# Kernel optimization log

Hardware: AMD Instinct MI355X
Metric: run time of the kernel (lower is better)

## Reference

```python
import jax, jax.numpy as jnp
import numpy as np
from jax import lax

DT = 1.0 / 120.0
B, T = 4096, 128
TWO_PI = 2.0 * np.pi


def setup_inputs() -> dict:
    key = jax.random.key(0)
    k1, k2, k3, k4 = jax.random.split(key, 4)
    return {
        "params": jax.random.normal(k1, (4,), jnp.float32),
        "covariance_params": jax.random.normal(k2, (7,), jnp.float32),
        "init_states": jax.random.normal(k3, (B, 6), jnp.float32),
        "measurements": jax.random.normal(k4, (B, T, 3), jnp.float32),
    }


def _wrap(a):
    # wrap angle innovation to [-pi, pi]
    return a - TWO_PI * jnp.round(a / TWO_PI)


def _smooth_loss(params, covariance_params, init_state, z):
    # z: [T, 3] measurements of (x, y, theta)
    friction = (jnp.tanh(params[0]) + 1.0) * 0.01
    damping = (jnp.tanh(params[1]) + 1.0) * 0.01
    cp = jax.nn.sigmoid(covariance_params)
    R = jnp.diag(cp[:3])                                    # [3,3] meas noise
    Q = jnp.diag(cp[jnp.array([3, 3, 4, 4, 5, 6])])         # [6,6] proc noise
    I6 = jnp.eye(6, dtype=z.dtype)
    Hm = jnp.zeros((3, 6), z.dtype).at[0, 0].set(1.).at[1, 1].set(1.).at[2, 4].set(1.)
    P0 = 0.01 * I6

    def f_and_F(s):
        # free-sliding puck dynamics: [x, y, dx, dy, th, dth]
        x, y, dx, dy, th, dth = s
        ndx = dx - DT * (damping * dx + friction * jnp.tanh(100. * dx))
        ndy = dy - DT * (damping * dy + friction * jnp.tanh(100. * dy))
        ndth = dth * (1.0 - DT * damping)
        ns = jnp.stack([x + DT * dx, y + DT * dy, ndx, ndy, th + DT * dth, ndth])
        gx = 1.0 - DT * (damping + friction * 100. * (1. - jnp.tanh(100. * dx) ** 2))
        gy = 1.0 - DT * (damping + friction * 100. * (1. - jnp.tanh(100. * dy) ** 2))
        F = (I6.at[0, 2].set(DT).at[1, 3].set(DT).at[4, 5].set(DT)
               .at[2, 2].set(gx).at[3, 3].set(gy).at[5, 5].set(1.0 - DT * damping))
        return ns, F

    def ekf_step(carry, zt):
        s, P = carry
        sp, F = f_and_F(s)
        Pp = F @ P @ F.T + Q
        S = Hm @ Pp @ Hm.T + R
        innov = zt - Hm @ sp
        innov = innov.at[2].set(_wrap(innov[2]))
        K = jnp.linalg.solve(S, Hm @ Pp).T          # Pp H^T S^-1
        s_new = sp + K @ innov
        P_new = (I6 - K @ Hm) @ Pp
        return (s_new, P_new), (s_new, P_new, sp, Pp, F)

    _, (sf, Pf, sp, Pp, Fs) = lax.scan(ekf_step, (init_state, P0), z)

    # RTS backward pass
    def rts_step(carry, inp):
        s_next, P_next = carry
        s_f, P_f, sp_n, Pp_n, F_n = inp
        G = jnp.linalg.solve(Pp_n, F_n @ P_f).T     # P_f F^T Pp^{-1}
        s_s = s_f + G @ (s_next - sp_n)
        P_s = P_f + G @ (P_next - Pp_n) @ G.T
        return (s_s, P_s), (s_s, P_s)

    inp = (sf[:-1], Pf[:-1], sp[1:], Pp[1:], Fs[1:])
    _, (s_sm_head, P_sm_head) = lax.scan(rts_step, (sf[-1], Pf[-1]), inp, reverse=True)
    s_sm = jnp.concatenate([s_sm_head, sf[-1:]], 0)   # [T,6]
    P_sm = jnp.concatenate([P_sm_head, Pf[-1:]], 0)   # [T,6,6]

    # log-lik style loss vs measurements[2:] (as in compute_loss)
    zz, st, Pt = z[2:], s_sm[2:], P_sm[2:]
    Sv = jnp.einsum('ij,tjk,lk->til', Hm, Pt, Hm) + R  # [T-2,3,3] meas-space var
    innov_xy = zz[:, :2] - st[:, :2]
    a = zz[:, 2] - st[:, 4]
    a = jnp.where(a > 1.5 * np.pi, a - TWO_PI, a)
    a = jnp.where(a < -1.5 * np.pi, a + TWO_PI, a)
    innov = jnp.concatenate([innov_xy, a[:, None]], 1)
    sign, logdet = jnp.linalg.slogdet(Sv)
    return jnp.sum(sign * jnp.exp(logdet) + jnp.einsum('ti,tij,tj->t', innov, Sv, innov))


def reference(params, covariance_params, init_states, measurements):
    per_seg = jax.vmap(_smooth_loss, in_axes=(None, None, 0, 0))(
        params, covariance_params, init_states, measurements)
    return jnp.sum(per_seg)
```

## Files before the change

kernel.cpp:

```cpp
#include <hip/hip_runtime.h>
#include <cmath>


namespace {

constexpr int B = 4096;
constexpr int T = 128;
constexpr int NT = B * 3;
constexpr int CPB = 64;
constexpr int NBLK = NT / CPB;
constexpr int RBLK = 512;
constexpr int RTH = 256;

constexpr float DTc     = 1.0f / 120.0f;
constexpr float TWO_PIc = 6.28318530717958647692f;
constexpr float PI_1_5  = 4.71238898038468985769f;
constexpr float INV_2PI = 0.15915494309189533577f;

__device__ __forceinline__ float frcp(float x) { return __builtin_amdgcn_rcpf(x); }

__device__ __forceinline__ float fast_tanh(float x) {
  float e = __expf(2.0f * x);
  return 1.0f - 2.0f * frcp(e + 1.0f);
}
__device__ __forceinline__ float sigmoidf(float x) {
  return frcp(1.0f + __expf(-x));
}

__global__ __launch_bounds__(256) void ztrans_kernel(
    const float* __restrict__ z, float* __restrict__ zt) {
  __shared__ float tile[96 * 65];
  const int tid = threadIdx.x;
  const int bs = blockIdx.x & 63;
  const int bt = blockIdx.x >> 6;
  const int s0 = bs * 64, t0 = bt * 32;

  const float* __restrict__ zbase = z + (size_t)s0 * 384 + t0 * 3;
#pragma unroll
  for (int k = 0; k < 6; k++) {
    const int idx = tid + k * 256;
    const int sl = idx / 24;
    const int c4 = idx - sl * 24;
    const float4 v4 = *(const float4*)(zbase + (size_t)sl * 384 + c4 * 4);
    tile[(c4 * 4 + 0) * 65 + sl] = v4.x;
    tile[(c4 * 4 + 1) * 65 + sl] = v4.y;
    tile[(c4 * 4 + 2) * 65 + sl] = v4.z;
    tile[(c4 * 4 + 3) * 65 + sl] = v4.w;
  }
  __syncthreads();
#pragma unroll
  for (int k = 0; k < 24; k++) {
    const int idx = tid + k * 256;
    const int r  = idx >> 6;
    const int sl = idx & 63;
    const int fc = r >> 5;
    const int tl = r & 31;
    zt[((size_t)fc * T + t0 + tl) * B + s0 + sl] = tile[(tl * 3 + fc) * 65 + sl];
  }
}

__global__ __launch_bounds__(CPB, 1) void filt_kernel(
    const float* __restrict__ params, const float* __restrict__ covp,
    const float* __restrict__ init_states, const float* __restrict__ zt,
    float4* __restrict__ tvg4, float2* __restrict__ aq) {
  const int lane = threadIdx.x;
  const int blk  = blockIdx.x;
  const int f    = blk >> 6;
  const int seq  = ((blk & 63) << 6) + lane;
  const int gid  = blk * CPB + lane;

  __shared__ float4 h4s[127 * CPB];
  __shared__ float  p11s[T * CPB];

  const float friction = (fast_tanh(params[0]) + 1.0f) * 0.01f;
  const float damping  = (fast_tanh(params[1]) + 1.0f) * 0.01f;
  float cp[7];
#pragma unroll
  for (int i = 0; i < 7; i++) cp[i] = sigmoidf(covp[i]);
  const float dcoef = 1.0f - DTc * damping;
  const bool isTH = (f == 2);
  const float q0 = isTH ? cp[5] : cp[3];
  const float q1 = isTH ? cp[6] : cp[4];
  const float r  = cp[f];

  const int pidx = (f == 0) ? 0 : (f == 1) ? 1 : 4;
  const int vidx = (f == 0) ? 2 : (f == 1) ? 3 : 5;
  float p = init_states[seq * 6 + pidx];
  float v = init_states[seq * 6 + vidx];
  float P00 = 0.01f, P01 = 0.0f, P11 = 0.01f;

  const float* __restrict__ ztf = zt + (size_t)f * T * B + seq;

  float zr[8];
#pragma unroll
  for (int k = 0; k < 8; k++) zr[k] = ztf[(size_t)k * B];
  float zlast = 0.0f;

#define FWD_BODY(t, REFILL)                                                  \
  {                                                                          \
    const float zc = zr[(t) & 7];                                            \
    if (REFILL) zr[(t) & 7] = ztf[(size_t)((t) + 8) * B];                    \
    float g, tv;                                                             \
    if (!isTH) {                                                             \
      const float th = fast_tanh(100.0f * v);                                \
      tv = v - DTc * (damping * v + friction * th);                          \
      g = 1.0f - DTc * (damping + 100.0f * friction * (1.0f - th * th));     \
    } else {                                                                 \
      tv = dcoef * v;                                                        \
      g = dcoef;                                                             \
    }                                                                        \
    const float tp = p + DTc * v;                                            \
    const float u = P01 + DTc * P11;                                         \
    const float Pp00 = P00 + DTc * P01 + DTc * u + q0;                       \
    const float Pp01 = g * u;                                                \
    const float Pp11 = g * (g * P11) + q1;                                   \
    tvg4[(size_t)(t) * NT + gid] = make_float4(tv, g, Pp00, Pp11);           \
    const float iS = frcp(Pp00 + r);                                         \
    const float K0 = Pp00 * iS;                                              \
    const float K1 = Pp01 * iS;                                              \
    float e = zc - tp;                                                       \
    if (isTH) e = e - TWO_PIc * rintf(e * INV_2PI);                          \
    p = tp + K0 * e;                                                         \
    v = tv + K1 * e;                                                         \
    const float om = 1.0f - K0;                                              \
    P00 = om * Pp00;                                                         \
    P01 = om * Pp01;                                                         \
    P11 = Pp11 - K1 * Pp01;                                                  \
    if ((t) < 127) h4s[(t) * CPB + lane] = make_float4(p, v, P00, P01);      \
    p11s[(t) * CPB + lane] = P11;                                            \
    if ((t) == 127) zlast = zc;                                              \
  }

#pragma unroll 8
  for (int t = 0; t < 120; t++) FWD_BODY(t, true)
#pragma unroll
  for (int t = 120; t < 128; t++) FWD_BODY(t, false)
#undef FWD_BODY

  {
    float e = zlast - p;
    if (isTH) {
      if (e >  PI_1_5) e -= TWO_PIc;
      if (e < -PI_1_5) e += TWO_PIc;
    }
    const float a = P00 + r;
    aq[((size_t)f * T + (T - 1)) * B + seq] = make_float2(a, a * e * e);
  }

  float sp_ = p, sv_ = v, Ps00 = P00, Ps01 = P01, Ps11 = P11;

  float4 h4r[4], dvr[4];
  float  p11r[4];
  float  zrb[8];
#pragma unroll
  for (int k = 0; k < 4; k++) {
    h4r[k]  = h4s[(126 - k) * CPB + lane];
    p11r[k] = p11s[(126 - k) * CPB + lane];
    dvr[k]  = tvg4[(size_t)(127 - k) * NT + gid];
  }
#pragma unroll
  for (int k = 0; k < 8; k++) zrb[k] = ztf[(size_t)(126 - k) * B];

#define BWD_BODY(i, RH4, RDV, RZ)                                            \
  {                                                                          \
    const int n = 126 - (i);                                                 \
    const float4 h4 = h4r[(i) & 3];                                          \
    const float f11 = p11r[(i) & 3];                                         \
    const float4 d4 = dvr[(i) & 3];                                          \
    const float zn_ = zrb[(i) & 7];                                          \
    if (RH4) {                                                               \
      const int nl = (n >= 6) ? n - 4 : 2;                                   \
      h4r[(i) & 3]  = h4s[nl * CPB + lane];                                  \
      p11r[(i) & 3] = p11s[nl * CPB + lane];                                 \
    }                                                                        \
    if (RDV) {                                                               \
      const int nd = (n >= 6) ? n - 3 : 3;                                   \
      dvr[(i) & 3] = tvg4[(size_t)nd * NT + gid];                            \
    }                                                                        \
    if (RZ) {                                                                \
      const int nz = (n >= 10) ? n - 8 : 2;                                  \
      zrb[(i) & 7] = ztf[(size_t)nz * B];                                    \
    }                                                                        \
    const float fp = h4.x, fv = h4.y, f00 = h4.z, f01 = h4.w;                \
    const float tv = d4.x, g = d4.y, Pp00 = d4.z, Pp11 = d4.w;               \
    const float tp = fp + DTc * fv;                                          \
    const float u = f01 + DTc * f11;                                         \
    const float Pp01 = g * u;                                                \
    const float dett = Pp00 * Pp11 - Pp01 * Pp01;                            \
    const float idet = frcp(dett);                                           \
    const float c0 = Pp11 * idet, c1 = Pp01 * idet, c2 = Pp00 * idet;        \
    const float W01 = DTc * f00 + g * f01;                                   \
    const float W11 = DTc * f01 + g * f11;                                   \
    const float G00 = f00 * c0 - W01 * c1;                                   \
    const float G01 = W01 * c2 - f00 * c1;                                   \
    const float G10 = f01 * c0 - W11 * c1;                                   \
    const float G11 = W11 * c2 - f01 * c1;                                   \
    const float ds0 = sp_ - tp, ds1 = sv_ - tv;                              \
    const float np = fp + G00 * ds0 + G01 * ds1;                             \
    const float nv = fv + G10 * ds0 + G11 * ds1;                             \
    const float M00 = Ps00 - Pp00, M01 = Ps01 - Pp01, M11 = Ps11 - Pp11;     \
    const float GM00 = G00 * M00 + G01 * M01, GM01 = G00 * M01 + G01 * M11;  \
    const float GM10 = G10 * M00 + G11 * M01, GM11 = G10 * M01 + G11 * M11;  \
    Ps00 = f00 + GM00 * G00 + GM01 * G01;                                    \
    Ps01 = f01 + GM00 * G10 + GM01 * G11;                                    \
    Ps11 = f11 + GM10 * G10 + GM11 * G11;                                    \
    sp_ = np;                                                                \
    sv_ = nv;                                                                \
    const float a = Ps00 + r;                                                \
    float e = zn_ - np;                                                      \
    if (isTH) {                                                              \
      if (e >  PI_1_5) e -= TWO_PIc;                                         \
      if (e < -PI_1_5) e += TWO_PIc;                                         \
    }                                                                        \
    aq[((size_t)f * T + n) * B + seq] = make_float2(a, a * e * e);           \
  }

#pragma unroll 8
  for (int i = 0; i < 112; i++) BWD_BODY(i, true, true, true)
#pragma unroll
  for (int i = 112; i < 125; i++)
    BWD_BODY(i, (126 - i) >= 6, (126 - i) >= 6, (126 - i) >= 10)
#undef BWD_BODY
}

__global__ __launch_bounds__(RTH) void reduce_kernel(
    const float4* __restrict__ aq4, float* __restrict__ out) {
  const int tid = threadIdx.x;
  constexpr int HB = B / 2;
  constexpr int NTERM4 = 126 * HB;
  float part = 0.0f;
  for (int idx = blockIdx.x * RTH + tid; idx < NTERM4; idx += RTH * RBLK) {
    const int t = 2 + (idx >> 11);
    const int s4 = idx & (HB - 1);
    const float4 a0 = aq4[((size_t)0 * T + t) * HB + s4];
    const float4 a1 = aq4[((size_t)1 * T + t) * HB + s4];
    const float4 a2 = aq4[((size_t)2 * T + t) * HB + s4];
    part += a0.x * a1.x * a2.x + (a0.y + a1.y + a2.y);
    part += a0.z * a1.z * a2.z + (a0.w + a1.w + a2.w);
  }
#pragma unroll
  for (int off = 32; off > 0; off >>= 1) part += __shfl_down(part, off);
  __shared__ float red[RTH / 64];
  if ((tid & 63) == 0) red[tid >> 6] = part;
  __syncthreads();
  if (tid == 0) {
    float s = 0.0f;
#pragma unroll
    for (int w = 0; w < RTH / 64; w++) s += red[w];
    atomicAdd(out, s);
  }
}

}

extern "C" void kernel_launch(void* const* d_in, const int* in_sizes, int n_in,
                              void* d_out, int out_size, void* d_ws, size_t ws_size,
                              hipStream_t stream) {
  const float* params      = (const float*)d_in[0];
  const float* covp        = (const float*)d_in[1];
  const float* init_states = (const float*)d_in[2];
  const float* z           = (const float*)d_in[3];
  float* out = (float*)d_out;

  const size_t ztB   = (size_t)T * NT * sizeof(float);
  const size_t aqB   = (size_t)T * NT * sizeof(float2);
  const size_t tvgB  = (size_t)T * NT * sizeof(float4);
  const size_t needBytes = ztB + aqB + tvgB;

  hipMemsetAsync(d_out, 0, sizeof(float), stream);

  if (ws_size >= needBytes) {
    float*  ztp  = (float*)d_ws;
    float2* aqp  = (float2*)((char*)d_ws + ztB);
    float4* tvgp = (float4*)((char*)d_ws + ztB + aqB);
    ztrans_kernel<<<256, 256, 0, stream>>>(z, ztp);
    filt_kernel<<<NBLK, CPB, 0, stream>>>(params, covp, init_states, ztp,
                                          tvgp, aqp);
    reduce_kernel<<<RBLK, RTH, 0, stream>>>((const float4*)aqp, out);
  }
}
```

Baseline: 126.2 us.

## Recompute predicted covariance in RTS pass instead of storing it to global memory

The forward filter no longer writes per-step predicted velocity, Jacobian and predicted covariance (a float4 per sequence per step) to a global workspace. The backward smoother now recomputes them from the filtered state already kept in shared memory, trading extra arithmetic (a tanh per step) for dropping a large global write and read stream. The separate memset of the output is also folded into the transpose kernel, which removes one launch. The backward-pass reload index clamping is simplified as well.

New measurement: 122.4 us. 3.0% less time.

```diff
diff --git a/kernel.cpp b/kernel.cpp
--- a/kernel.cpp
+++ b/kernel.cpp
@@ -28,9 +28,11 @@
 }
 
 __global__ __launch_bounds__(256) void ztrans_kernel(
-    const float* __restrict__ z, float* __restrict__ zt) {
+    const float* __restrict__ z, float* __restrict__ zt,
+    float* __restrict__ out) {
   __shared__ float tile[96 * 65];
   const int tid = threadIdx.x;
+  if (blockIdx.x == 0 && tid == 0) out[0] = 0.0f;
   const int bs = blockIdx.x & 63;
   const int bt = blockIdx.x >> 6;
   const int s0 = bs * 64, t0 = bt * 32;
@@ -62,12 +64,11 @@
 __global__ __launch_bounds__(CPB, 1) void filt_kernel(
     const float* __restrict__ params, const float* __restrict__ covp,
     const float* __restrict__ init_states, const float* __restrict__ zt,
-    float4* __restrict__ tvg4, float2* __restrict__ aq) {
+    float2* __restrict__ aq) {
   const int lane = threadIdx.x;
   const int blk  = blockIdx.x;
   const int f    = blk >> 6;
   const int seq  = ((blk & 63) << 6) + lane;
-  const int gid  = blk * CPB + lane;
 
   __shared__ float4 h4s[127 * CPB];
   __shared__ float  p11s[T * CPB];
@@ -114,7 +115,6 @@
     const float Pp00 = P00 + DTc * P01 + DTc * u + q0;                       \
     const float Pp01 = g * u;                                                \
     const float Pp11 = g * (g * P11) + q1;                                   \
-    tvg4[(size_t)(t) * NT + gid] = make_float4(tv, g, Pp00, Pp11);           \
     const float iS = frcp(Pp00 + r);                                         \
     const float K0 = Pp00 * iS;                                              \
     const float K1 = Pp01 * iS;                                              \
@@ -149,52 +149,50 @@
 
   float sp_ = p, sv_ = v, Ps00 = P00, Ps01 = P01, Ps11 = P11;
 
-  float4 h4r[4], dvr[4];
+  float4 h4r[4];
   float  p11r[4];
   float  zrb[8];
 #pragma unroll
   for (int k = 0; k < 4; k++) {
     h4r[k]  = h4s[(126 - k) * CPB + lane];
     p11r[k] = p11s[(126 - k) * CPB + lane];
-    dvr[k]  = tvg4[(size_t)(127 - k) * NT + gid];
   }
 #pragma unroll
   for (int k = 0; k < 8; k++) zrb[k] = ztf[(size_t)(126 - k) * B];
 
-#define BWD_BODY(i, RH4, RDV, RZ)                                            \
+#define BWD_BODY(i, RH4, RZ)                                                 \
   {                                                                          \
     const int n = 126 - (i);                                                 \
     const float4 h4 = h4r[(i) & 3];                                          \
     const float f11 = p11r[(i) & 3];                                         \
-    const float4 d4 = dvr[(i) & 3];                                          \
     const float zn_ = zrb[(i) & 7];                                          \
     if (RH4) {                                                               \
-      const int nl = (n >= 6) ? n - 4 : 2;                                   \
-      h4r[(i) & 3]  = h4s[nl * CPB + lane];                                  \
-      p11r[(i) & 3] = p11s[nl * CPB + lane];                                 \
-    }                                                                        \
-    if (RDV) {                                                               \
-      const int nd = (n >= 6) ? n - 3 : 3;                                   \
-      dvr[(i) & 3] = tvg4[(size_t)nd * NT + gid];                            \
-    }                                                                        \
-    if (RZ) {                                                                \
-      const int nz = (n >= 10) ? n - 8 : 2;                                  \
-      zrb[(i) & 7] = ztf[(size_t)nz * B];                                    \
-    }                                                                        \
+      h4r[(i) & 3]  = h4s[(n - 4) * CPB + lane];                             \
+      p11r[(i) & 3] = p11s[(n - 4) * CPB + lane];                            \
+    }                                                                        \
+    if (RZ) zrb[(i) & 7] = ztf[(size_t)(n - 8) * B];                         \
     const float fp = h4.x, fv = h4.y, f00 = h4.z, f01 = h4.w;                \
-    const float tv = d4.x, g = d4.y, Pp00 = d4.z, Pp11 = d4.w;               \
+    float g, tv;                                                             \
+    if (!isTH) {                                                             \
+      const float th = fast_tanh(100.0f * fv);                               \
+      tv = fv - DTc * (damping * fv + friction * th);                        \
+      g = 1.0f - DTc * (damping + 100.0f * friction * (1.0f - th * th));     \
+    } else {                                                                 \
+      tv = dcoef * fv;                                                       \
+      g = dcoef;                                                             \
+    }                                                                        \
     const float tp = fp + DTc * fv;                                          \
     const float u = f01 + DTc * f11;                                         \
+    const float Pp00 = f00 + DTc * f01 + DTc * u + q0;                       \
     const float Pp01 = g * u;                                                \
-    const float dett = Pp00 * Pp11 - Pp01 * Pp01;                            \
-    const float idet = frcp(dett);                                           \
-    const float c0 = Pp11 * idet, c1 = Pp01 * idet, c2 = Pp00 * idet;        \
-    const float W01 = DTc * f00 + g * f01;                                   \
-    const float W11 = DTc * f01 + g * f11;                                   \
-    const float G00 = f00 * c0 - W01 * c1;                                   \
-    const float G01 = W01 * c2 - f00 * c1;                                   \
-    const float G10 = f01 * c0 - W11 * c1;                                   \
-    const float G11 = W11 * c2 - f01 * c1;                                   \
+    const float Pp11 = g * (g * f11) + q1;                                   \
+    const float idet = frcp(Pp00 * Pp11 - Pp01 * Pp01);                      \
+    const float W00 = f00, W01 = DTc * f00 + g * f01;                        \
+    const float W10 = f01, W11 = DTc * f01 + g * f11;                        \
+    const float G00 = (W00 * Pp11 - W01 * Pp01) * idet;                      \
+    const float G01 = (W01 * Pp00 - W00 * Pp01) * idet;                      \
+    const float G10 = (W10 * Pp11 - W11 * Pp01) * idet;                      \
+    const float G11 = (W11 * Pp00 - W10 * Pp01) * idet;                      \
     const float ds0 = sp_ - tp, ds1 = sv_ - tv;                              \
     const float np = fp + G00 * ds0 + G01 * ds1;                             \
     const float nv = fv + G10 * ds0 + G11 * ds1;                             \
@@ -216,10 +214,10 @@
   }
 
 #pragma unroll 8
-  for (int i = 0; i < 112; i++) BWD_BODY(i, true, true, true)
+  for (int i = 0; i < 112; i++) BWD_BODY(i, true, true)
 #pragma unroll
   for (int i = 112; i < 125; i++)
-    BWD_BODY(i, (126 - i) >= 6, (126 - i) >= 6, (126 - i) >= 10)
+    BWD_BODY(i, (126 - i) >= 6, (126 - i) >= 10)
 #undef BWD_BODY
 }
 
@@ -262,20 +260,17 @@
   const float* z           = (const float*)d_in[3];
   float* out = (float*)d_out;
 
-  const size_t ztB   = (size_t)T * NT * sizeof(float);
-  const size_t aqB   = (size_t)T * NT * sizeof(float2);
-  const size_t tvgB  = (size_t)T * NT * sizeof(float4);
-  const size_t needBytes = ztB + aqB + tvgB;
-
-  hipMemsetAsync(d_out, 0, sizeof(float), stream);
+  const size_t ztB = (size_t)T * NT * sizeof(float);
+  const size_t aqB = (size_t)T * NT * sizeof(float2);
+  const size_t needBytes = ztB + aqB;
 
   if (ws_size >= needBytes) {
-    float*  ztp  = (float*)d_ws;
-    float2* aqp  = (float2*)((char*)d_ws + ztB);
-    float4* tvgp = (float4*)((char*)d_ws + ztB + aqB);
-    ztrans_kernel<<<256, 256, 0, stream>>>(z, ztp);
-    filt_kernel<<<NBLK, CPB, 0, stream>>>(params, covp, init_states, ztp,
-                                          tvgp, aqp);
+    float*  ztp = (float*)d_ws;
+    float2* aqp = (float2*)((char*)d_ws + ztB);
+    ztrans_kernel<<<256, 256, 0, stream>>>(z, ztp, out);
+    filt_kernel<<<NBLK, CPB, 0, stream>>>(params, covp, init_states, ztp, aqp);
     reduce_kernel<<<RBLK, RTH, 0, stream>>>((const float4*)aqp, out);
-  }
-}
+  } else {
+    hipMemsetAsync(d_out, 0, sizeof(float), stream);
+  }
+}
```
